# Kernel optimization log

Hardware: AMD Instinct MI355X
Metric: run time of the kernel (lower is better)

## Reference

```python
import jax, jax.numpy as jnp
import numpy as np

B, NQ, NK, D, H = 2, 1024, 2048, 1024, 16
HD = D // H
SCALE = HD ** -0.5


def setup_inputs() -> dict:
    key = jax.random.key(0)
    ks = jax.random.split(key, 14)
    inp = {
        "query": jax.random.normal(ks[0], (B, NQ, D), jnp.float32),
        "key": jax.random.normal(ks[1], (B, NK, D), jnp.float32),
        "value": jax.random.normal(ks[2], (B, NK, D), jnp.float32),
        "attn_bias": jax.random.normal(ks[3], (B, H, NQ, NK), jnp.float32) * 0.1,
        "key_padding_mask": jax.random.bernoulli(ks[4], 0.1, (B, NK)),  # True = masked
    }
    s = D ** -0.5
    inp["Wq"] = jax.random.normal(ks[5], (D, D), jnp.float32) * s
    inp["bq"] = jnp.zeros((D,), jnp.float32)
    inp["Wk"] = jax.random.normal(ks[6], (D, D), jnp.float32) * s
    inp["bk"] = jnp.zeros((D,), jnp.float32)
    inp["Wv"] = jax.random.normal(ks[7], (D, D), jnp.float32) * s
    inp["bv"] = jnp.zeros((D,), jnp.float32)
    inp["Wo"] = jax.random.normal(ks[8], (D, D), jnp.float32) * s
    inp["bo"] = jnp.zeros((D,), jnp.float32)
    return inp


def reference(query, key, value, attn_bias, key_padding_mask, Wq, bq, Wk, bk, Wv, bv, Wo, bo):
    b, nq, d = query.shape
    nk = key.shape[1]
    # projections -> [b, H, n, hd]
    q = (query @ Wq + bq).reshape(b, nq, H, HD).transpose(0, 2, 1, 3)
    k = (key @ Wk + bk).reshape(b, nk, H, HD).transpose(0, 2, 1, 3)
    v = (value @ Wv + bv).reshape(b, nk, H, HD).transpose(0, 2, 1, 3)
    logits = jnp.einsum("bhqd,bhkd->bhqk", q, k) * SCALE + attn_bias
    # safe mask: if an entire row is masked, unmask position 0 to avoid NaNs
    all_masked = jnp.all(key_padding_mask, axis=1)  # [b]
    safe_mask = key_padding_mask.at[:, 0].set(
        jnp.where(all_masked, False, key_padding_mask[:, 0]))
    logits = jnp.where(safe_mask[:, None, None, :], -jnp.inf, logits)
    attn = jax.nn.softmax(logits, axis=-1)  # dropout p=0.0 -> identity
    out = jnp.einsum("bhqk,bhkd->bhqd", attn, v)
    out = out.transpose(0, 2, 1, 3).reshape(b, nq, d)
    return out @ Wo + bo
```

## Files before the change

kernel.cpp:

```cpp
#include <hip/hip_runtime.h>
#include <stdint.h>
#include <math.h>

typedef unsigned short ushort_t;
typedef short bf16x8 __attribute__((ext_vector_type(8)));
typedef float f32x4  __attribute__((ext_vector_type(4)));

#define B_   2
#define NQ_  1024
#define NK_  2048
#define D_   1024
#define H_   16
#define HD_  64

__device__ __forceinline__ ushort_t f2b(float f) {
  union { float f; unsigned int i; } x; x.f = f;
  unsigned int r = (x.i + 0x7FFFu + ((x.i >> 16) & 1u)) >> 16;
  return (ushort_t)r;
}
__device__ __forceinline__ void g2l16(const void* g, void* l) {
  __builtin_amdgcn_global_load_lds(
      (const __attribute__((address_space(1))) unsigned int*)g,
      (__attribute__((address_space(3))) unsigned int*)l, 16, 0, 0);
}
__device__ __forceinline__ f32x4 mfma16(bf16x8 a, bf16x8 b, f32x4 c) {
  return __builtin_amdgcn_mfma_f32_16x16x32_bf16(a, b, c, 0, 0, 0);
}

template <bool A_F32, bool C_F32>
__global__ __launch_bounds__(256) void gemm_bt(
    const void* __restrict__ Av, const ushort_t* __restrict__ Bt,
    const float* __restrict__ bias, void* __restrict__ Cv,
    int M, float alpha)
{
  constexpr int N = 1024, K = 1024, BK = 64;
  __shared__ __align__(16) ushort_t As[128 * BK];
  __shared__ __align__(16) ushort_t Bs[128 * BK];
  const int tid  = threadIdx.x;
  const int wid  = tid >> 6, lane = tid & 63;
  const int quad = lane >> 4, l15 = lane & 15;
  const int m0 = blockIdx.y * 128, n0 = blockIdx.x * 128;
  const int wm = (wid & 1) * 64,  wn = (wid >> 1) * 64;
  const int srow = tid >> 3, scol = (tid & 7) * 8;

  const float*    Af = (const float*)Av;
  const ushort_t* Ab = (const ushort_t*)Av;
  const ushort_t* bBase = Bt + (size_t)(n0 + srow) * K + scol;
  ushort_t* asDst = As + tid * 8;
  ushort_t* bsDst = Bs + tid * 8;

  f32x4 acc[4][4];
#pragma unroll
  for (int i = 0; i < 4; i++)
#pragma unroll
    for (int j = 0; j < 4; j++) { f32x4 z = {0.f,0.f,0.f,0.f}; acc[i][j] = z; }

  for (int k0 = 0; k0 < K; k0 += BK) {
    __syncthreads();
#pragma unroll
    for (int j = 0; j < 4; j++)
      g2l16(bBase + (size_t)j * 32 * K + k0, bsDst + j * 2048);
    if constexpr (A_F32) {
#pragma unroll
      for (int j = 0; j < 4; j++) {
        const float* p = Af + (size_t)(m0 + srow + j * 32) * K + k0 + scol;
        float4 x = *(const float4*)p;
        float4 y = *(const float4*)(p + 4);
        bf16x8 v;
        ((ushort_t*)&v)[0] = f2b(x.x); ((ushort_t*)&v)[1] = f2b(x.y);
        ((ushort_t*)&v)[2] = f2b(x.z); ((ushort_t*)&v)[3] = f2b(x.w);
        ((ushort_t*)&v)[4] = f2b(y.x); ((ushort_t*)&v)[5] = f2b(y.y);
        ((ushort_t*)&v)[6] = f2b(y.z); ((ushort_t*)&v)[7] = f2b(y.w);
        *(bf16x8*)(asDst + j * 2048) = v;
      }
    } else {
#pragma unroll
      for (int j = 0; j < 4; j++)
        g2l16(Ab + (size_t)(m0 + srow + j * 32) * K + k0 + scol, asDst + j * 2048);
    }
    asm volatile("s_waitcnt vmcnt(0)" ::: "memory");
    __syncthreads();
#pragma unroll
    for (int ks = 0; ks < 2; ks++) {
      bf16x8 af[4], bfr[4];
#pragma unroll
      for (int t = 0; t < 4; t++) {
        af[t]  = *(const bf16x8*)(As + (wm + t * 16 + l15) * BK + ks * 32 + quad * 8);
        bfr[t] = *(const bf16x8*)(Bs + (wn + t * 16 + l15) * BK + ks * 32 + quad * 8);
      }
#pragma unroll
      for (int mt = 0; mt < 4; mt++)
#pragma unroll
        for (int nt = 0; nt < 4; nt++)
          acc[mt][nt] = mfma16(af[mt], bfr[nt], acc[mt][nt]);
    }
  }
  float bn[4];
#pragma unroll
  for (int nt = 0; nt < 4; nt++) bn[nt] = bias[n0 + wn + nt * 16 + l15];
#pragma unroll
  for (int mt = 0; mt < 4; mt++) {
    const int mb = m0 + wm + mt * 16 + quad * 4;
#pragma unroll
    for (int nt = 0; nt < 4; nt++) {
      const int n = n0 + wn + nt * 16 + l15;
#pragma unroll
      for (int r = 0; r < 4; r++) {
        const float val = (acc[mt][nt][r] + bn[nt]) * alpha;
        if constexpr (C_F32) ((float*)Cv)[(size_t)(mb + r) * N + n] = val;
        else ((ushort_t*)Cv)[(size_t)(mb + r) * N + n] = f2b(val);
      }
    }
  }
}

struct WTP { const float* src[4]; ushort_t* dst[4]; };

__global__ __launch_bounds__(256) void wtrans_k(WTP p) {
  constexpr int Kd = 1024, Nd = 1024;
  __shared__ ushort_t t[64][72];
  const float* X = p.src[blockIdx.z];
  ushort_t*    Y = p.dst[blockIdx.z];
  const int rt = blockIdx.y * 64, ct = blockIdx.x * 64;
  const int tid = threadIdx.x;
  const int lr = tid >> 3, lc = (tid & 7) * 8;
#pragma unroll
  for (int j = 0; j < 2; j++) {
    const float* px = X + (size_t)(rt + j * 32 + lr) * Nd + ct + lc;
    float4 x = *(const float4*)px;
    float4 y = *(const float4*)(px + 4);
    ushort_t* tr = &t[j * 32 + lr][lc];
    tr[0] = f2b(x.x); tr[1] = f2b(x.y); tr[2] = f2b(x.z); tr[3] = f2b(x.w);
    tr[4] = f2b(y.x); tr[5] = f2b(y.y); tr[6] = f2b(y.z); tr[7] = f2b(y.w);
  }
  __syncthreads();
#pragma unroll
  for (int j = 0; j < 2; j++) {
    bf16x8 w;
#pragma unroll
    for (int i = 0; i < 8; i++) ((ushort_t*)&w)[i] = t[lc + i][j * 32 + lr];
    *(bf16x8*)(Y + (size_t)(ct + j * 32 + lr) * Kd + rt + lc) = w;
  }
}

struct TPtrs { const ushort_t* src[2]; ushort_t* dst[2]; };

__global__ __launch_bounds__(256) void vtrans_k(TPtrs p, int R, int C) {
  __shared__ ushort_t t[64][68];
  const ushort_t* X = p.src[blockIdx.z];
  ushort_t*       Y = p.dst[blockIdx.z];
  const int rt = blockIdx.y * 64, ct = blockIdx.x * 64;
  const int tid = threadIdx.x;
  const int lr = tid >> 3, lc = (tid & 7) * 8;
#pragma unroll
  for (int j = 0; j < 2; j++) {
    bf16x8 v = *(const bf16x8*)(X + (size_t)(rt + j * 32 + lr) * C + ct + lc);
#pragma unroll
    for (int i = 0; i < 8; i++) t[j * 32 + lr][lc + i] = ((ushort_t*)&v)[i];
  }
  __syncthreads();
#pragma unroll
  for (int j = 0; j < 2; j++) {
    bf16x8 w;
#pragma unroll
    for (int i = 0; i < 8; i++) ((ushort_t*)&w)[i] = t[lc + i][j * 32 + lr];
    *(bf16x8*)(Y + (size_t)(ct + j * 32 + lr) * R + rt + lc) = w;
  }
}

__global__ __launch_bounds__(256) void mask_prep(const unsigned char* __restrict__ mraw,
                                                 float* __restrict__ maskf, int n) {
  __shared__ int is_u8;
  const int tid = threadIdx.x;
  if (tid == 0) is_u8 = 0;
  __syncthreads();
  int nz = 0;
  for (int i = tid; i < n; i += 256)
    if ((i & 3) != 0 && mraw[i] != 0) nz = 1;
  if (nz) is_u8 = 1;
  __syncthreads();
  const int u8 = is_u8;
  const int* mi = (const int*)mraw;
  for (int k = tid; k < n; k += 256) {
    int v = u8 ? (int)mraw[k] : mi[k];
    maskf[k] = v ? -1e30f : 0.0f;
  }
}

__global__ __launch_bounds__(256) void flash_attn(
    const ushort_t* __restrict__ Qp, const ushort_t* __restrict__ Kp,
    const ushort_t* __restrict__ Vt, const float* __restrict__ bias,
    const float* __restrict__ maskf, ushort_t* __restrict__ Ao)
{
  __shared__ __align__(16) ushort_t Ks[64 * 64];
  __shared__ __align__(16) ushort_t Vs[64 * 64];
  __shared__ __align__(16) ushort_t Ps[4][16 * 64];
  const int b = blockIdx.z, h = blockIdx.y, q0 = blockIdx.x * 64;
  const int tid  = threadIdx.x, wid = tid >> 6, lane = tid & 63;
  const int quad = lane >> 4, l15 = lane & 15;
  const int qw   = q0 + wid * 16;
  const int srow = tid >> 3, scol = (tid & 7) * 8;

  bf16x8 qf[2];
#pragma unroll
  for (int ks = 0; ks < 2; ks++)
    qf[ks] = *(const bf16x8*)(Qp + (size_t)(b * NQ_ + qw + l15) * D_ + h * HD_ + ks * 32 + quad * 8);

  f32x4 o[4];
#pragma unroll
  for (int nt = 0; nt < 4; nt++) { f32x4 z = {0.f,0.f,0.f,0.f}; o[nt] = z; }
  float mrow[4] = {-INFINITY, -INFINITY, -INFINITY, -INFINITY};
  float lrow[4] = {0.f, 0.f, 0.f, 0.f};

  const float*    biasBase = bias + ((size_t)(b * H_ + h) * NQ_ + qw) * NK_;
  const float*    mBase    = maskf + b * NK_;
  const ushort_t* kBase    = Kp + (size_t)(b * NK_ + srow) * D_ + h * HD_ + scol;
  const ushort_t* vBase    = Vt + (size_t)(b * D_ + h * HD_ + srow) * NK_ + scol;

  for (int k0 = 0; k0 < NK_; k0 += 64) {
    __syncthreads();
#pragma unroll
    for (int j = 0; j < 2; j++) {
      g2l16(kBase + (size_t)(k0 + j * 32) * D_, Ks + tid * 8 + j * 2048);
      g2l16(vBase + (size_t)j * 32 * NK_ + k0, Vs + tid * 8 + j * 2048);
    }
    asm volatile("s_waitcnt vmcnt(0)" ::: "memory");
    __syncthreads();

    f32x4 s[4];
#pragma unroll
    for (int nt = 0; nt < 4; nt++) { f32x4 z = {0.f,0.f,0.f,0.f}; s[nt] = z; }
#pragma unroll
    for (int ks = 0; ks < 2; ks++)
#pragma unroll
      for (int nt = 0; nt < 4; nt++) {
        bf16x8 kf = *(const bf16x8*)(Ks + (nt * 16 + l15) * 64 + ks * 32 + quad * 8);
        s[nt] = mfma16(qf[ks], kf, s[nt]);
      }

    float z[4][4];
#pragma unroll
    for (int nt = 0; nt < 4; nt++) {
      const float mk = mBase[k0 + nt * 16 + l15];
#pragma unroll
      for (int r = 0; r < 4; r++)
        z[nt][r] = s[nt][r] + biasBase[(size_t)(quad * 4 + r) * NK_ + k0 + nt * 16 + l15] + mk;
    }

    float alpha_[4];
#pragma unroll
    for (int r = 0; r < 4; r++) {
      float v = fmaxf(fmaxf(z[0][r], z[1][r]), fmaxf(z[2][r], z[3][r]));
      v = fmaxf(v, __shfl_xor(v, 1)); v = fmaxf(v, __shfl_xor(v, 2));
      v = fmaxf(v, __shfl_xor(v, 4)); v = fmaxf(v, __shfl_xor(v, 8));
      float mn = fmaxf(mrow[r], v);
      alpha_[r] = __expf(mrow[r] - mn);
      mrow[r] = mn;
    }
    float rsum[4] = {0.f, 0.f, 0.f, 0.f};
#pragma unroll
    for (int nt = 0; nt < 4; nt++)
#pragma unroll
      for (int r = 0; r < 4; r++) {
        float p = __expf(z[nt][r] - mrow[r]);
        rsum[r] += p;
        Ps[wid][(quad * 4 + r) * 64 + nt * 16 + l15] = f2b(p);
      }
#pragma unroll
    for (int r = 0; r < 4; r++) {
      float v = rsum[r];
      v += __shfl_xor(v, 1); v += __shfl_xor(v, 2);
      v += __shfl_xor(v, 4); v += __shfl_xor(v, 8);
      lrow[r] = lrow[r] * alpha_[r] + v;
    }
#pragma unroll
    for (int nt = 0; nt < 4; nt++) {
      f32x4 t = o[nt];
#pragma unroll
      for (int r = 0; r < 4; r++) t[r] *= alpha_[r];
      o[nt] = t;
    }
#pragma unroll
    for (int ks = 0; ks < 2; ks++) {
      bf16x8 pa = *(const bf16x8*)(&Ps[wid][l15 * 64 + ks * 32 + quad * 8]);
#pragma unroll
      for (int nt = 0; nt < 4; nt++) {
        bf16x8 vf = *(const bf16x8*)(Vs + (nt * 16 + l15) * 64 + ks * 32 + quad * 8);
        o[nt] = mfma16(pa, vf, o[nt]);
      }
    }
  }
#pragma unroll
  for (int nt = 0; nt < 4; nt++)
#pragma unroll
    for (int r = 0; r < 4; r++)
      Ao[(size_t)(b * NQ_ + qw + quad * 4 + r) * D_ + h * HD_ + nt * 16 + l15]
          = f2b(o[nt][r] / lrow[r]);
}

extern "C" void kernel_launch(void* const* d_in, const int* in_sizes, int n_in,
                              void* d_out, int out_size, void* d_ws, size_t ws_size,
                              hipStream_t stream)
{
  const float* query = (const float*)d_in[0];
  const float* key   = (const float*)d_in[1];
  const float* value = (const float*)d_in[2];
  const float* abias = (const float*)d_in[3];
  const unsigned char* mask = (const unsigned char*)d_in[4];
  const float* Wq = (const float*)d_in[5];
  const float* bq = (const float*)d_in[6];
  const float* Wk = (const float*)d_in[7];
  const float* bk = (const float*)d_in[8];
  const float* Wv = (const float*)d_in[9];
  const float* bv = (const float*)d_in[10];
  const float* Wo = (const float*)d_in[11];
  const float* bo = (const float*)d_in[12];
  float* out = (float*)d_out;

  char* ws = (char*)d_ws;
  const size_t MB = 1ull << 20;
  ushort_t* WqT   = (ushort_t*)(ws + 0 * MB);
  ushort_t* WkT   = (ushort_t*)(ws + 2 * MB);
  ushort_t* WvT   = (ushort_t*)(ws + 4 * MB);
  ushort_t* WoT   = (ushort_t*)(ws + 6 * MB);
  float*    maskf = (float*)   (ws + 8 * MB);
  ushort_t* Qp    = (ushort_t*)(ws + 9 * MB);
  ushort_t* Kp    = (ushort_t*)(ws + 13 * MB);
  ushort_t* Vp    = (ushort_t*)(ws + 21 * MB);
  ushort_t* Vt    = (ushort_t*)(ws + 29 * MB);
  ushort_t* Ao    = (ushort_t*)(ws + 37 * MB);

  WTP wt; wt.src[0] = Wq; wt.src[1] = Wk; wt.src[2] = Wv; wt.src[3] = Wo;
  wt.dst[0] = WqT; wt.dst[1] = WkT; wt.dst[2] = WvT; wt.dst[3] = WoT;
  wtrans_k<<<dim3(16, 16, 4), 256, 0, stream>>>(wt);

  mask_prep<<<1, 256, 0, stream>>>(mask, maskf, B_ * NK_);

  gemm_bt<true, false><<<dim3(8, 16), 256, 0, stream>>>(query, WqT, bq, Qp, B_ * NQ_, 0.125f);
  gemm_bt<true, false><<<dim3(8, 32), 256, 0, stream>>>(key,   WkT, bk, Kp, B_ * NK_, 1.0f);
  gemm_bt<true, false><<<dim3(8, 32), 256, 0, stream>>>(value, WvT, bv, Vp, B_ * NK_, 1.0f);

  TPtrs vt; vt.src[0] = Vp; vt.src[1] = Vp + (size_t)NK_ * D_;
  vt.dst[0] = Vt; vt.dst[1] = Vt + (size_t)D_ * NK_;
  vtrans_k<<<dim3(16, 32, 2), 256, 0, stream>>>(vt, NK_, D_);

  flash_attn<<<dim3(NQ_ / 64, H_, B_), 256, 0, stream>>>(Qp, Kp, Vt, abias, maskf, Ao);

  gemm_bt<false, true><<<dim3(8, 16), 256, 0, stream>>>(Ao, WoT, bo, out, B_ * NQ_, 1.0f);
}
```

Before: 592.0 us.

## Fuse QKV projections into one launch, stage bias via LDS, cheaper bf16 rounding

Merges the three Q/K/V projection GEMMs into a single grid so the small Q launch no longer underfills the GPU and two launches go away. In flash attention, the per-tile attention bias is loaded asynchronously into LDS together with K/V, replacing strided scalar global loads. Round-to-nearest-even bf16 conversion is replaced with a simpler add-and-shift rounding on packed words, which rounds ties differently. The added 16KB LDS buffer may lower flash-attention occupancy.

```diff
diff --git a/kernel.cpp b/kernel.cpp
--- a/kernel.cpp
+++ b/kernel.cpp
@@ -18,6 +18,10 @@
   unsigned int r = (x.i + 0x7FFFu + ((x.i >> 16) & 1u)) >> 16;
   return (ushort_t)r;
 }
+__device__ __forceinline__ ushort_t f2b_fast(float f) {
+  union { float f; unsigned int i; } x; x.f = f;
+  return (ushort_t)((x.i + 0x8000u) >> 16);
+}
 __device__ __forceinline__ void g2l16(const void* g, void* l) {
   __builtin_amdgcn_global_load_lds(
       (const __attribute__((address_space(1))) unsigned int*)g,
@@ -28,10 +32,10 @@
 }
 
 template <bool A_F32, bool C_F32>
-__global__ __launch_bounds__(256) void gemm_bt(
+__device__ __forceinline__ void gemm_tile(
     const void* __restrict__ Av, const ushort_t* __restrict__ Bt,
     const float* __restrict__ bias, void* __restrict__ Cv,
-    int M, float alpha)
+    int m0, int n0, float alpha)
 {
   constexpr int N = 1024, K = 1024, BK = 64;
   __shared__ __align__(16) ushort_t As[128 * BK];
@@ -39,7 +43,6 @@
   const int tid  = threadIdx.x;
   const int wid  = tid >> 6, lane = tid & 63;
   const int quad = lane >> 4, l15 = lane & 15;
-  const int m0 = blockIdx.y * 128, n0 = blockIdx.x * 128;
   const int wm = (wid & 1) * 64,  wn = (wid >> 1) * 64;
   const int srow = tid >> 3, scol = (tid & 7) * 8;
 
@@ -63,15 +66,15 @@
     if constexpr (A_F32) {
 #pragma unroll
       for (int j = 0; j < 4; j++) {
-        const float* p = Af + (size_t)(m0 + srow + j * 32) * K + k0 + scol;
-        float4 x = *(const float4*)p;
-        float4 y = *(const float4*)(p + 4);
-        bf16x8 v;
-        ((ushort_t*)&v)[0] = f2b(x.x); ((ushort_t*)&v)[1] = f2b(x.y);
-        ((ushort_t*)&v)[2] = f2b(x.z); ((ushort_t*)&v)[3] = f2b(x.w);
-        ((ushort_t*)&v)[4] = f2b(y.x); ((ushort_t*)&v)[5] = f2b(y.y);
-        ((ushort_t*)&v)[6] = f2b(y.z); ((ushort_t*)&v)[7] = f2b(y.w);
-        *(bf16x8*)(asDst + j * 2048) = v;
+        const unsigned* p = (const unsigned*)(Af + (size_t)(m0 + srow + j * 32) * K + k0 + scol);
+        uint4 x = *(const uint4*)p;
+        uint4 y = *(const uint4*)(p + 4);
+        uint4 o;
+        o.x = ((x.y + 0x8000u) & 0xFFFF0000u) | ((x.x + 0x8000u) >> 16);
+        o.y = ((x.w + 0x8000u) & 0xFFFF0000u) | ((x.z + 0x8000u) >> 16);
+        o.z = ((y.y + 0x8000u) & 0xFFFF0000u) | ((y.x + 0x8000u) >> 16);
+        o.w = ((y.w + 0x8000u) & 0xFFFF0000u) | ((y.z + 0x8000u) >> 16);
+        *(uint4*)(asDst + j * 2048) = o;
       }
     } else {
 #pragma unroll
@@ -108,10 +111,29 @@
       for (int r = 0; r < 4; r++) {
         const float val = (acc[mt][nt][r] + bn[nt]) * alpha;
         if constexpr (C_F32) ((float*)Cv)[(size_t)(mb + r) * N + n] = val;
-        else ((ushort_t*)Cv)[(size_t)(mb + r) * N + n] = f2b(val);
-      }
-    }
-  }
+        else ((ushort_t*)Cv)[(size_t)(mb + r) * N + n] = f2b_fast(val);
+      }
+    }
+  }
+}
+
+struct Proj3P {
+  const float* A[3]; const ushort_t* Bt[3]; const float* bias[3];
+  ushort_t* C[3]; float alpha[3];
+};
+
+__global__ __launch_bounds__(256) void proj3_k(Proj3P p) {
+  const int y = blockIdx.y;
+  const int i = (y < 16) ? 0 : (y < 48 ? 1 : 2);
+  const int my = y - ((i == 0) ? 0 : (i == 1) ? 16 : 48);
+  gemm_tile<true, false>(p.A[i], p.Bt[i], p.bias[i], p.C[i],
+                         my * 128, blockIdx.x * 128, p.alpha[i]);
+}
+
+__global__ __launch_bounds__(256) void gemm_out_k(
+    const ushort_t* __restrict__ A, const ushort_t* __restrict__ Bt,
+    const float* __restrict__ bias, float* __restrict__ C) {
+  gemm_tile<false, true>(A, Bt, bias, C, blockIdx.y * 128, blockIdx.x * 128, 1.0f);
 }
 
 struct WTP { const float* src[4]; ushort_t* dst[4]; };
@@ -195,6 +217,7 @@
   __shared__ __align__(16) ushort_t Ks[64 * 64];
   __shared__ __align__(16) ushort_t Vs[64 * 64];
   __shared__ __align__(16) ushort_t Ps[4][16 * 64];
+  __shared__ __align__(16) float    Bf[64 * 64];
   const int b = blockIdx.z, h = blockIdx.y, q0 = blockIdx.x * 64;
   const int tid  = threadIdx.x, wid = tid >> 6, lane = tid & 63;
   const int quad = lane >> 4, l15 = lane & 15;
@@ -212,10 +235,12 @@
   float mrow[4] = {-INFINITY, -INFINITY, -INFINITY, -INFINITY};
   float lrow[4] = {0.f, 0.f, 0.f, 0.f};
 
-  const float*    biasBase = bias + ((size_t)(b * H_ + h) * NQ_ + qw) * NK_;
+  const float*    biasBase = bias + ((size_t)(b * H_ + h) * NQ_ + q0) * NK_;
   const float*    mBase    = maskf + b * NK_;
   const ushort_t* kBase    = Kp + (size_t)(b * NK_ + srow) * D_ + h * HD_ + scol;
   const ushort_t* vBase    = Vt + (size_t)(b * D_ + h * HD_ + srow) * NK_ + scol;
+  const int bRow0 = wid * 16 + (lane >> 4);
+  const int bCol  = (l15) * 4;
 
   for (int k0 = 0; k0 < NK_; k0 += 64) {
     __syncthreads();
@@ -224,6 +249,10 @@
       g2l16(kBase + (size_t)(k0 + j * 32) * D_, Ks + tid * 8 + j * 2048);
       g2l16(vBase + (size_t)j * 32 * NK_ + k0, Vs + tid * 8 + j * 2048);
     }
+#pragma unroll
+    for (int j = 0; j < 4; j++)
+      g2l16(biasBase + (size_t)(bRow0 + j * 4) * NK_ + k0 + bCol,
+            (char*)Bf + (wid * 16 + j * 4) * 256);
     asm volatile("s_waitcnt vmcnt(0)" ::: "memory");
     __syncthreads();
 
@@ -244,7 +273,7 @@
       const float mk = mBase[k0 + nt * 16 + l15];
 #pragma unroll
       for (int r = 0; r < 4; r++)
-        z[nt][r] = s[nt][r] + biasBase[(size_t)(quad * 4 + r) * NK_ + k0 + nt * 16 + l15] + mk;
+        z[nt][r] = s[nt][r] + Bf[(wid * 16 + quad * 4 + r) * 64 + nt * 16 + l15] + mk;
     }
 
     float alpha_[4];
@@ -264,7 +293,7 @@
       for (int r = 0; r < 4; r++) {
         float p = __expf(z[nt][r] - mrow[r]);
         rsum[r] += p;
-        Ps[wid][(quad * 4 + r) * 64 + nt * 16 + l15] = f2b(p);
+        Ps[wid][(quad * 4 + r) * 64 + nt * 16 + l15] = f2b_fast(p);
       }
 #pragma unroll
     for (int r = 0; r < 4; r++) {
@@ -295,7 +324,7 @@
 #pragma unroll
     for (int r = 0; r < 4; r++)
       Ao[(size_t)(b * NQ_ + qw + quad * 4 + r) * D_ + h * HD_ + nt * 16 + l15]
-          = f2b(o[nt][r] / lrow[r]);
+          = f2b_fast(o[nt][r] / lrow[r]);
 }
 
 extern "C" void kernel_launch(void* const* d_in, const int* in_sizes, int n_in,
@@ -336,9 +365,13 @@
 
   mask_prep<<<1, 256, 0, stream>>>(mask, maskf, B_ * NK_);
 
-  gemm_bt<true, false><<<dim3(8, 16), 256, 0, stream>>>(query, WqT, bq, Qp, B_ * NQ_, 0.125f);
-  gemm_bt<true, false><<<dim3(8, 32), 256, 0, stream>>>(key,   WkT, bk, Kp, B_ * NK_, 1.0f);
-  gemm_bt<true, false><<<dim3(8, 32), 256, 0, stream>>>(value, WvT, bv, Vp, B_ * NK_, 1.0f);
+  Proj3P pp;
+  pp.A[0] = query; pp.A[1] = key; pp.A[2] = value;
+  pp.Bt[0] = WqT;  pp.Bt[1] = WkT; pp.Bt[2] = WvT;
+  pp.bias[0] = bq; pp.bias[1] = bk; pp.bias[2] = bv;
+  pp.C[0] = Qp;    pp.C[1] = Kp;   pp.C[2] = Vp;
+  pp.alpha[0] = 0.125f; pp.alpha[1] = 1.0f; pp.alpha[2] = 1.0f;
+  proj3_k<<<dim3(8, 80), 256, 0, stream>>>(pp);
 
   TPtrs vt; vt.src[0] = Vp; vt.src[1] = Vp + (size_t)NK_ * D_;
   vt.dst[0] = Vt; vt.dst[1] = Vt + (size_t)D_ * NK_;
@@ -346,5 +379,5 @@
 
   flash_attn<<<dim3(NQ_ / 64, H_, B_), 256, 0, stream>>>(Qp, Kp, Vt, abias, maskf, Ao);
 
-  gemm_bt<false, true><<<dim3(8, 16), 256, 0, stream>>>(Ao, WoT, bo, out, B_ * NQ_, 1.0f);
-}
+  gemm_out_k<<<dim3(8, 16), 256, 0, stream>>>(Ao, WoT, bo, out);
+}
```

Result: faster. 569.5 us (-3.8%).
